# Optimization experiments

Measured on AMD Instinct MI355X. Metric: run time of the kernel, lower is better.

## Reference

```python
import jax, jax.numpy as jnp
import numpy as np

N_NODES = 50000
N_EDGES = 800000
D_IN = 512
D_OUT = 512


def setup_inputs() -> dict:
    key = jax.random.key(0)
    k1, k2, k3, k4, k5 = jax.random.split(key, 5)
    x = jax.random.normal(k1, (N_NODES, D_IN), dtype=jnp.float32)
    weight = jax.random.normal(k2, (D_IN, D_OUT), dtype=jnp.float32) * (1.0 / np.sqrt(D_IN))
    edge_weight = jax.random.uniform(k3, (N_EDGES,), dtype=jnp.float32)
    edge_src = jax.random.randint(k4, (N_EDGES,), 0, N_NODES, dtype=jnp.int32)
    edge_dst = jax.random.randint(k5, (N_EDGES,), 0, N_NODES, dtype=jnp.int32)
    return {"x": x, "weight": weight, "edge_weight": edge_weight,
            "edge_src": edge_src, "edge_dst": edge_dst}


def reference(x, weight, edge_weight, edge_src, edge_dst):
    # support = x @ W  (dense GEMM, [N, D_out])
    support = jnp.matmul(x, weight)
    # output = adj @ support  (SpMM in COO form):
    # gather source rows, scale by edge weight, scatter-add into destinations
    msgs = support[edge_src] * edge_weight[:, None]          # [E, D_out]
    output = jax.ops.segment_sum(msgs, edge_dst, num_segments=N_NODES)
    return output
```

## Files before the change

kernel.cpp:

```cpp
#include <hip/hip_runtime.h>
#include <stdint.h>

#define N_NODES 50000
#define N_EDGES 800000
#define D 512
#define M_PAD 50048
#define SCAN_NB 196

typedef __attribute__((ext_vector_type(8))) __bf16 bf16x8;
typedef __attribute__((ext_vector_type(4))) float f32x4;

static __device__ __forceinline__ unsigned short f2bf(float f) {
  unsigned u = __float_as_uint(f);
  u += 0x7fff + ((u >> 16) & 1);
  return (unsigned short)(u >> 16);
}
static __device__ __forceinline__ float bf2f(unsigned short h) {
  return __uint_as_float(((unsigned)h) << 16);
}

__global__ void k_cvt_x(const float* __restrict__ x, unsigned short* __restrict__ xb) {
  long long base = ((long long)blockIdx.x * blockDim.x + threadIdx.x) * 4;
  if (base >= (long long)M_PAD * D) return;
  int row = (int)(base >> 9);
  ushort4 o;
  if (row < N_NODES) {
    float4 v = *(const float4*)(x + base);
    o.x = f2bf(v.x); o.y = f2bf(v.y); o.z = f2bf(v.z); o.w = f2bf(v.w);
  } else {
    o.x = 0; o.y = 0; o.z = 0; o.w = 0;
  }
  *(ushort4*)(xb + base) = o;
}

__global__ void k_cvt_wt(const float* __restrict__ w, unsigned short* __restrict__ wt) {
  int k = blockIdx.x;
  int n = threadIdx.x;
  wt[n * D + k] = f2bf(w[k * D + n]);
}

__global__ __launch_bounds__(256) void k_gemm(const unsigned short* __restrict__ A,
                                              const unsigned short* __restrict__ Bt,
                                              unsigned short* __restrict__ C) {
  __shared__ unsigned short lds_a[128 * 32];
  __shared__ unsigned short lds_b[128 * 32];
  const int tid  = threadIdx.x;
  const int bm   = blockIdx.x >> 2;
  const int bn   = blockIdx.x & 3;
  const int m0   = bm * 128, n0 = bn * 128;
  const int wave = tid >> 6, lane = tid & 63;
  const int wm   = wave & 1, wn = wave >> 1;
  const int l15  = lane & 15, quad = lane >> 4;

  f32x4 acc[4][4];
#pragma unroll
  for (int i = 0; i < 4; i++)
#pragma unroll
    for (int j = 0; j < 4; j++) acc[i][j] = f32x4{0.f, 0.f, 0.f, 0.f};

  for (int kt = 0; kt < D / 32; ++kt) {
    const int k0 = kt * 32;
    __syncthreads();
#pragma unroll
    for (int c = 0; c < 2; c++) {
      int i = tid + c * 256;
      int r = i >> 2, kc = (i & 3) << 3;
      *(uint4*)&lds_a[i << 3] = *(const uint4*)&A[(long long)(m0 + r) * D + k0 + kc];
      *(uint4*)&lds_b[i << 3] = *(const uint4*)&Bt[(n0 + r) * D + k0 + kc];
    }
    __syncthreads();
    bf16x8 af[4], bfr[4];
#pragma unroll
    for (int t = 0; t < 4; t++) {
      af[t]  = *(const bf16x8*)&lds_a[(wm * 64 + t * 16 + l15) * 32 + quad * 8];
      bfr[t] = *(const bf16x8*)&lds_b[(wn * 64 + t * 16 + l15) * 32 + quad * 8];
    }
#pragma unroll
    for (int i = 0; i < 4; i++)
#pragma unroll
      for (int j = 0; j < 4; j++)
        acc[i][j] = __builtin_amdgcn_mfma_f32_16x16x32_bf16(af[i], bfr[j], acc[i][j], 0, 0, 0);
  }
#pragma unroll
  for (int i = 0; i < 4; i++)
#pragma unroll
    for (int j = 0; j < 4; j++)
#pragma unroll
      for (int r = 0; r < 4; r++) {
        int row = m0 + wm * 64 + i * 16 + quad * 4 + r;
        int col = n0 + wn * 64 + j * 16 + l15;
        C[(long long)row * D + col] = f2bf(acc[i][j][r]);
      }
}

__global__ void k_zero(int* deg) {
  int i = blockIdx.x * 256 + threadIdx.x;
  if (i < N_NODES) deg[i] = 0;
}
__global__ void k_hist(const int* __restrict__ dst, int* deg) {
  int e = blockIdx.x * 256 + threadIdx.x;
  if (e < N_EDGES) atomicAdd(&deg[dst[e]], 1);
}

__global__ void k_scan1(const int* __restrict__ deg, int* __restrict__ bsum) {
  __shared__ int red[256];
  int i = blockIdx.x * 256 + threadIdx.x;
  red[threadIdx.x] = (i < N_NODES) ? deg[i] : 0;
  __syncthreads();
#pragma unroll
  for (int s = 128; s > 0; s >>= 1) {
    if ((int)threadIdx.x < s) red[threadIdx.x] += red[threadIdx.x + s];
    __syncthreads();
  }
  if (threadIdx.x == 0) bsum[blockIdx.x] = red[0];
}
__global__ void k_scan2(int* __restrict__ bsum) {
  __shared__ int tmp[256];
  int t = threadIdx.x;
  int v = (t < SCAN_NB) ? bsum[t] : 0;
  tmp[t] = v;
  __syncthreads();
#pragma unroll
  for (int s = 1; s < 256; s <<= 1) {
    int add = (t >= s) ? tmp[t - s] : 0;
    __syncthreads();
    tmp[t] += add;
    __syncthreads();
  }
  if (t < SCAN_NB) bsum[t] = tmp[t] - v;
}
__global__ void k_scan3(const int* __restrict__ deg, const int* __restrict__ bsum,
                        int* __restrict__ off, int* __restrict__ cur) {
  __shared__ int tmp[256];
  int t = threadIdx.x, i = blockIdx.x * 256 + t;
  int v = (i < N_NODES) ? deg[i] : 0;
  tmp[t] = v;
  __syncthreads();
#pragma unroll
  for (int s = 1; s < 256; s <<= 1) {
    int add = (t >= s) ? tmp[t - s] : 0;
    __syncthreads();
    tmp[t] += add;
    __syncthreads();
  }
  int pre = tmp[t] - v + bsum[blockIdx.x];
  if (i < N_NODES) {
    off[i] = pre;
    cur[i] = pre;
    if (i == N_NODES - 1) off[N_NODES] = pre + v;
  }
}

__global__ void k_fill(const int* __restrict__ src, const int* __restrict__ dst,
                       const float* __restrict__ w, int* cur,
                       int* __restrict__ csrc, float* __restrict__ cw) {
  int e = blockIdx.x * 256 + threadIdx.x;
  if (e >= N_EDGES) return;
  int d = dst[e];
  int p = atomicAdd(&cur[d], 1);
  csrc[p] = src[e];
  cw[p]   = w[e];
}

__global__ __launch_bounds__(256) void k_agg(const int* __restrict__ off, const int* __restrict__ csrc,
                                             const float* __restrict__ cw,
                                             const unsigned short* __restrict__ S,
                                             float* __restrict__ out) {
  __shared__ int   s_src[256];
  __shared__ float s_w[256];
  int node  = blockIdx.x;
  int start = off[node], end = off[node + 1];
  int col   = threadIdx.x * 2;
  float a0 = 0.f, a1 = 0.f;
  for (int cs = start; cs < end; cs += 256) {
    int n = min(256, end - cs);
    if ((int)threadIdx.x < n) {
      s_src[threadIdx.x] = csrc[cs + threadIdx.x];
      s_w[threadIdx.x]   = cw[cs + threadIdx.x];
    }
    __syncthreads();
    int i = 0;
    for (; i + 4 <= n; i += 4) {
      unsigned v0 = *(const unsigned*)(S + (long long)s_src[i + 0] * D + col);
      unsigned v1 = *(const unsigned*)(S + (long long)s_src[i + 1] * D + col);
      unsigned v2 = *(const unsigned*)(S + (long long)s_src[i + 2] * D + col);
      unsigned v3 = *(const unsigned*)(S + (long long)s_src[i + 3] * D + col);
      float w0 = s_w[i], w1 = s_w[i + 1], w2 = s_w[i + 2], w3 = s_w[i + 3];
      a0 = fmaf(w0, bf2f((unsigned short)(v0 & 0xffffu)), a0);
      a1 = fmaf(w0, bf2f((unsigned short)(v0 >> 16)), a1);
      a0 = fmaf(w1, bf2f((unsigned short)(v1 & 0xffffu)), a0);
      a1 = fmaf(w1, bf2f((unsigned short)(v1 >> 16)), a1);
      a0 = fmaf(w2, bf2f((unsigned short)(v2 & 0xffffu)), a0);
      a1 = fmaf(w2, bf2f((unsigned short)(v2 >> 16)), a1);
      a0 = fmaf(w3, bf2f((unsigned short)(v3 & 0xffffu)), a0);
      a1 = fmaf(w3, bf2f((unsigned short)(v3 >> 16)), a1);
    }
    for (; i < n; i++) {
      unsigned v = *(const unsigned*)(S + (long long)s_src[i] * D + col);
      float w = s_w[i];
      a0 = fmaf(w, bf2f((unsigned short)(v & 0xffffu)), a0);
      a1 = fmaf(w, bf2f((unsigned short)(v >> 16)), a1);
    }
    __syncthreads();
  }
  *(float2*)(out + (long long)node * D + col) = make_float2(a0, a1);
}

extern "C" void kernel_launch(void* const* d_in, const int* in_sizes, int n_in,
                              void* d_out, int out_size, void* d_ws, size_t ws_size,
                              hipStream_t stream) {
  const float* x    = (const float*)d_in[0];
  const float* w    = (const float*)d_in[1];
  const float* ew   = (const float*)d_in[2];
  const int*   esrc = (const int*)d_in[3];
  const int*   edst = (const int*)d_in[4];
  float* out = (float*)d_out;

  char* p = (char*)d_ws;
  auto align256 = [](size_t v) { return (v + 255) & ~(size_t)255; };
  unsigned short* xb = (unsigned short*)p;  p += align256((size_t)M_PAD * D * 2);
  unsigned short* sb = (unsigned short*)p;  p += align256((size_t)M_PAD * D * 2);
  unsigned short* wt = (unsigned short*)p;  p += align256((size_t)D * D * 2);
  int*   deg  = (int*)p;   p += align256((size_t)N_NODES * 4);
  int*   off  = (int*)p;   p += align256((size_t)(N_NODES + 1) * 4);
  int*   cur  = (int*)p;   p += align256((size_t)N_NODES * 4);
  int*   csrc = (int*)p;   p += align256((size_t)N_EDGES * 4);
  float* cw   = (float*)p; p += align256((size_t)N_EDGES * 4);
  int*   bsum = (int*)p;   p += align256((size_t)256 * 4);

  k_cvt_x<<<(M_PAD * D / 4 + 255) / 256, 256, 0, stream>>>(x, xb);
  k_cvt_wt<<<D, D, 0, stream>>>(w, wt);
  k_gemm<<<391 * 4, 256, 0, stream>>>(xb, wt, sb);
  k_zero<<<(N_NODES + 255) / 256, 256, 0, stream>>>(deg);
  k_hist<<<(N_EDGES + 255) / 256, 256, 0, stream>>>(edst, deg);
  k_scan1<<<SCAN_NB, 256, 0, stream>>>(deg, bsum);
  k_scan2<<<1, 256, 0, stream>>>(bsum);
  k_scan3<<<SCAN_NB, 256, 0, stream>>>(deg, bsum, off, cur);
  k_fill<<<(N_EDGES + 255) / 256, 256, 0, stream>>>(esrc, edst, ew, cur, csrc, cw);
  k_agg<<<N_NODES, 256, 0, stream>>>(off, csrc, cw, sb, out);
}
```

Before: 440.2 us.

## Use direct global-to-LDS loads in GEMM and split aggregation edges across waves

The GEMM tile staging now uses global_load_lds to copy 16-byte chunks straight into shared memory, with no pass through registers. The aggregation kernel is restructured so that each of the four waves handles a strided subset of edges. Each lane loads 16 bytes (8 bf16) per edge, with two edges in flight per iteration, and the per-wave partial sums are then reduced through LDS. The aim is wider memory transactions, more parallelism across edges, and fewer block-wide barriers in the SpMM. The cost is extra LDS traffic for the final reduction, plus reliance on the wave-uniform LDS base layout that global_load_lds requires.

```diff
diff --git a/kernel.cpp b/kernel.cpp
--- a/kernel.cpp
+++ b/kernel.cpp
@@ -17,6 +17,11 @@
 }
 static __device__ __forceinline__ float bf2f(unsigned short h) {
   return __uint_as_float(((unsigned)h) << 16);
+}
+
+static __device__ __forceinline__ void gload_lds16(const void* g, void* l) {
+  __builtin_amdgcn_global_load_lds((const __attribute__((address_space(1))) unsigned*)g,
+                                   (__attribute__((address_space(3))) unsigned*)l, 16, 0, 0);
 }
 
 __global__ void k_cvt_x(const float* __restrict__ x, unsigned short* __restrict__ xb) {
@@ -63,10 +68,10 @@
     __syncthreads();
 #pragma unroll
     for (int c = 0; c < 2; c++) {
-      int i = tid + c * 256;
+      int i = c * 256 + wave * 64 + lane;
       int r = i >> 2, kc = (i & 3) << 3;
-      *(uint4*)&lds_a[i << 3] = *(const uint4*)&A[(long long)(m0 + r) * D + k0 + kc];
-      *(uint4*)&lds_b[i << 3] = *(const uint4*)&Bt[(n0 + r) * D + k0 + kc];
+      gload_lds16(&A[(long long)(m0 + r) * D + k0 + kc], &lds_a[(c * 256 + wave * 64) * 8]);
+      gload_lds16(&Bt[(long long)(n0 + r) * D + k0 + kc], &lds_b[(c * 256 + wave * 64) * 8]);
     }
     __syncthreads();
     bf16x8 af[4], bfr[4];
@@ -166,44 +171,54 @@
                                              const float* __restrict__ cw,
                                              const unsigned short* __restrict__ S,
                                              float* __restrict__ out) {
-  __shared__ int   s_src[256];
-  __shared__ float s_w[256];
-  int node  = blockIdx.x;
-  int start = off[node], end = off[node + 1];
-  int col   = threadIdx.x * 2;
-  float a0 = 0.f, a1 = 0.f;
-  for (int cs = start; cs < end; cs += 256) {
-    int n = min(256, end - cs);
-    if ((int)threadIdx.x < n) {
-      s_src[threadIdx.x] = csrc[cs + threadIdx.x];
-      s_w[threadIdx.x]   = cw[cs + threadIdx.x];
-    }
-    __syncthreads();
-    int i = 0;
-    for (; i + 4 <= n; i += 4) {
-      unsigned v0 = *(const unsigned*)(S + (long long)s_src[i + 0] * D + col);
-      unsigned v1 = *(const unsigned*)(S + (long long)s_src[i + 1] * D + col);
-      unsigned v2 = *(const unsigned*)(S + (long long)s_src[i + 2] * D + col);
-      unsigned v3 = *(const unsigned*)(S + (long long)s_src[i + 3] * D + col);
-      float w0 = s_w[i], w1 = s_w[i + 1], w2 = s_w[i + 2], w3 = s_w[i + 3];
-      a0 = fmaf(w0, bf2f((unsigned short)(v0 & 0xffffu)), a0);
-      a1 = fmaf(w0, bf2f((unsigned short)(v0 >> 16)), a1);
-      a0 = fmaf(w1, bf2f((unsigned short)(v1 & 0xffffu)), a0);
-      a1 = fmaf(w1, bf2f((unsigned short)(v1 >> 16)), a1);
-      a0 = fmaf(w2, bf2f((unsigned short)(v2 & 0xffffu)), a0);
-      a1 = fmaf(w2, bf2f((unsigned short)(v2 >> 16)), a1);
-      a0 = fmaf(w3, bf2f((unsigned short)(v3 & 0xffffu)), a0);
-      a1 = fmaf(w3, bf2f((unsigned short)(v3 >> 16)), a1);
-    }
-    for (; i < n; i++) {
-      unsigned v = *(const unsigned*)(S + (long long)s_src[i] * D + col);
-      float w = s_w[i];
-      a0 = fmaf(w, bf2f((unsigned short)(v & 0xffffu)), a0);
-      a1 = fmaf(w, bf2f((unsigned short)(v >> 16)), a1);
-    }
-    __syncthreads();
-  }
-  *(float2*)(out + (long long)node * D + col) = make_float2(a0, a1);
+  __shared__ float s_part[4 * 512];
+  const int node  = blockIdx.x;
+  const int start = off[node], end = off[node + 1];
+  const int wave  = threadIdx.x >> 6, lane = threadIdx.x & 63;
+  float a[8];
+#pragma unroll
+  for (int k = 0; k < 8; k++) a[k] = 0.f;
+
+#define EDGE_FMA(V, W)                                             \
+  do {                                                             \
+    a[0] = fmaf(W, bf2f((unsigned short)(V.x & 0xffffu)), a[0]);   \
+    a[1] = fmaf(W, bf2f((unsigned short)(V.x >> 16)),     a[1]);   \
+    a[2] = fmaf(W, bf2f((unsigned short)(V.y & 0xffffu)), a[2]);   \
+    a[3] = fmaf(W, bf2f((unsigned short)(V.y >> 16)),     a[3]);   \
+    a[4] = fmaf(W, bf2f((unsigned short)(V.z & 0xffffu)), a[4]);   \
+    a[5] = fmaf(W, bf2f((unsigned short)(V.z >> 16)),     a[5]);   \
+    a[6] = fmaf(W, bf2f((unsigned short)(V.w & 0xffffu)), a[6]);   \
+    a[7] = fmaf(W, bf2f((unsigned short)(V.w >> 16)),     a[7]);   \
+  } while (0)
+
+  int e = start + wave;
+  for (; e + 4 < end; e += 8) {
+    int   s0 = csrc[e],     s1 = csrc[e + 4];
+    float w0 = cw[e],       w1 = cw[e + 4];
+    uint4 v0 = *(const uint4*)(S + (size_t)s0 * D + lane * 8);
+    uint4 v1 = *(const uint4*)(S + (size_t)s1 * D + lane * 8);
+    EDGE_FMA(v0, w0);
+    EDGE_FMA(v1, w1);
+  }
+  if (e < end) {
+    int   s0 = csrc[e];
+    float w0 = cw[e];
+    uint4 v0 = *(const uint4*)(S + (size_t)s0 * D + lane * 8);
+    EDGE_FMA(v0, w0);
+  }
+#undef EDGE_FMA
+
+  float4* sp = (float4*)&s_part[wave * 512 + lane * 8];
+  sp[0] = make_float4(a[0], a[1], a[2], a[3]);
+  sp[1] = make_float4(a[4], a[5], a[6], a[7]);
+  __syncthreads();
+  int col = threadIdx.x * 2;
+  float2 r0 = *(const float2*)&s_part[0 * 512 + col];
+  float2 r1 = *(const float2*)&s_part[1 * 512 + col];
+  float2 r2 = *(const float2*)&s_part[2 * 512 + col];
+  float2 r3 = *(const float2*)&s_part[3 * 512 + col];
+  *(float2*)(out + (size_t)node * D + col) =
+      make_float2(r0.x + r1.x + r2.x + r3.x, r0.y + r1.y + r2.y + r3.y);
 }
 
 extern "C" void kernel_launch(void* const* d_in, const int* in_sizes, int n_in,
```

After: 437.2 us. Within noise of the previous version (-0.7%).
